# Performance work log

Measured on AMD Instinct MI355X. Metric: run time of the kernel, lower is better.

Reference implementation:

```python
import jax, jax.numpy as jnp
import numpy as np

ALPHA = 0.2  # LeakyReLU negative slope
NEG_INF = -9e15

def setup_inputs() -> dict:
    key = jax.random.key(0)
    k1, k2, k3, k4 = jax.random.split(key, 4)
    N, F_in, F_out = 8192, 256, 64
    h = jax.random.normal(k1, (N, F_in), dtype=jnp.float32)
    adj = jax.random.randint(k2, (N, N), 0, 2, dtype=jnp.int32)
    # xavier_uniform with gain=1.414
    def xavier(k, shape, gain=1.414):
        fan_in, fan_out = shape[0], shape[1]
        limit = gain * np.sqrt(6.0 / (fan_in + fan_out))
        return jax.random.uniform(k, shape, jnp.float32, -limit, limit)
    W = xavier(k3, (F_in, F_out))
    a = xavier(k4, (2 * F_out, 1))
    return {"h": h, "adj": adj, "W": W, "a": a}

def reference(h, adj, W, a):
    # Wh: (N, F_out)
    Wh = h @ W
    F_out = Wh.shape[1]
    a1 = a[:F_out, 0]   # (F_out,)
    a2 = a[F_out:, 0]   # (F_out,)
    # e_ij = LeakyReLU(Wh_i . a1 + Wh_j . a2)  -- equivalent to a^T [Wh_i || Wh_j]
    e = jax.nn.leaky_relu((Wh @ a1)[:, None] + (Wh @ a2)[None, :], negative_slope=ALPHA)
    scores = jnp.where(adj > 0, e, NEG_INF)
    attention = jax.nn.softmax(scores, axis=1)  # (N, N)
    h_prime = attention @ Wh                    # (N, F_out)
    return jax.nn.elu(h_prime)  # concat=True path
```

## Files before the change

kernel.cpp:

```cpp
#include <hip/hip_runtime.h>
#include <hip/hip_bf16.h>

#define N 8192
#define FIN 256
#define FOUT 64
#define NSLICE 8
#define SLICE_J (N / NSLICE)
#define NEG_INF -9.0e15f
#define L2E 1.4426950408889634f

typedef __attribute__((ext_vector_type(8))) short short8;
typedef __attribute__((ext_vector_type(4))) float f32x4;

static __device__ __forceinline__ short f2bf(float v) {
    __hip_bfloat16 b = __float2bfloat16(v);
    return __builtin_bit_cast(short, b);
}
static __device__ __forceinline__ float bf2f(short s) {
    unsigned u = ((unsigned)(unsigned short)s) << 16;
    return __builtin_bit_cast(float, u);
}
static __device__ __forceinline__ float exp2fast(float x) {
    return __builtin_amdgcn_exp2f(x);
}

__global__ __launch_bounds__(256) void k_wh(const float* __restrict__ h,
                                            const float* __restrict__ W,
                                            const float* __restrict__ a,
                                            float* __restrict__ Wh,
                                            float* __restrict__ s1,
                                            float* __restrict__ s2) {
    int wave = threadIdx.x >> 6, lane = threadIdx.x & 63;
    int i = blockIdx.x * 4 + wave;
    const float* hrow = h + (size_t)i * FIN;
    float acc = 0.f;
#pragma unroll 8
    for (int k = 0; k < FIN; k += 4) {
        float4 hv = *(const float4*)(hrow + k);
        acc += hv.x * W[(k + 0) * FOUT + lane];
        acc += hv.y * W[(k + 1) * FOUT + lane];
        acc += hv.z * W[(k + 2) * FOUT + lane];
        acc += hv.w * W[(k + 3) * FOUT + lane];
    }
    Wh[(size_t)i * FOUT + lane] = acc;
    float v1 = acc * a[lane];
    float v2 = acc * a[FOUT + lane];
#pragma unroll
    for (int off = 32; off; off >>= 1) {
        v1 += __shfl_xor(v1, off);
        v2 += __shfl_xor(v2, off);
    }
    if (lane == 0) { s1[i] = v1 * L2E; s2[i] = v2 * L2E; }
}

__global__ __launch_bounds__(256) void k_max(const float* __restrict__ s2,
                                             float* __restrict__ maxs2) {
    int t = threadIdx.x;
    float m = NEG_INF;
    for (int i = t; i < N; i += 256) m = fmaxf(m, s2[i]);
#pragma unroll
    for (int off = 32; off; off >>= 1) m = fmaxf(m, __shfl_xor(m, off));
    __shared__ float red[4];
    if ((t & 63) == 0) red[t >> 6] = m;
    __syncthreads();
    if (t == 0) {
        float r = fmaxf(fmaxf(red[0], red[1]), fmaxf(red[2], red[3]));
        maxs2[0] = r;
    }
}

__global__ __launch_bounds__(256) void k_repack(const float* __restrict__ Wh,
                                                short* __restrict__ WhB) {
    int t = blockIdx.x * 256 + threadIdx.x;
    int lane = t & 63, ft = (t >> 6) & 3, jt = t >> 8;
    int g = lane >> 4, r = lane & 15;
    short8 w;
#pragma unroll
    for (int q = 0; q < 8; ++q) {
        float v = Wh[(size_t)(jt * 32 + g * 8 + q) * FOUT + ft * 16 + r];
        w[q] = f2bf(v);
    }
    *((short8*)WhB + t) = w;
}

__global__ __launch_bounds__(128) void k_flash(const int* __restrict__ adj,
                                               const short* __restrict__ WhB,
                                               const float* __restrict__ s1,
                                               const float* __restrict__ s2,
                                               const float* __restrict__ maxs2,
                                               float* __restrict__ pO,
                                               float* __restrict__ pl) {
    int rb = blockIdx.x / NSLICE, sl = blockIdx.x % NSLICE;
    int wave = threadIdx.x >> 6, lane = threadIdx.x & 63;
    int r = lane & 15, g = lane >> 4;
    int row = rb * 32 + wave * 16 + r;

    __shared__ __align__(16) float s2s[SLICE_J];
    for (int t = threadIdx.x; t < SLICE_J; t += 128) s2s[t] = s2[sl * SLICE_J + t];
    __syncthreads();

    unsigned long long chunks[16];
    {
        int rbase = rb * 32 + wave * 16;
        const int* abase = adj + (size_t)rbase * N + sl * SLICE_J;
        for (int i = 0; i < 16; ++i) {
            const int* ar = abase + (size_t)i * N;
#pragma unroll
            for (int w = 0; w < 16; ++w) {
                unsigned long long bal = __ballot(ar[w * 64 + lane] > 0);
                if (r == i) chunks[w] = bal;
            }
        }
    }

    float s1i = s1[row];
    float xm = s1i + maxs2[0];
    float Mp = fmaxf(xm, 0.2f * xm);

    float l = 0.f;
    f32x4 acc0 = {0.f, 0.f, 0.f, 0.f};
    f32x4 acc1 = {0.f, 0.f, 0.f, 0.f};
    f32x4 acc2 = {0.f, 0.f, 0.f, 0.f};
    f32x4 acc3 = {0.f, 0.f, 0.f, 0.f};

#pragma unroll
    for (int step = 0; step < SLICE_J / 32; ++step) {
        unsigned bits = (unsigned)((chunks[step >> 1] >>
                                    (((step & 1) << 5) + (g << 3))) & 0xffull);
        float4 sv0 = *(const float4*)&s2s[step * 32 + g * 8];
        float4 sv1 = *(const float4*)&s2s[step * 32 + g * 8 + 4];

        short8 af;
        auto pc = [&](unsigned bit, float s2v) -> short {
            float x = s1i + s2v;
            float lr = fmaxf(x, 0.2f * x);
            float p = exp2fast(lr - Mp);
            return bit ? f2bf(p) : (short)0;
        };
        af[0] = pc(bits & 1u, sv0.x);        af[1] = pc((bits >> 1) & 1u, sv0.y);
        af[2] = pc((bits >> 2) & 1u, sv0.z); af[3] = pc((bits >> 3) & 1u, sv0.w);
        af[4] = pc((bits >> 4) & 1u, sv1.x); af[5] = pc((bits >> 5) & 1u, sv1.y);
        af[6] = pc((bits >> 6) & 1u, sv1.z); af[7] = pc((bits >> 7) & 1u, sv1.w);

        l += bf2f(af[0]) + bf2f(af[1]) + bf2f(af[2]) + bf2f(af[3]) +
             bf2f(af[4]) + bf2f(af[5]) + bf2f(af[6]) + bf2f(af[7]);

        int jt = sl * (SLICE_J / 32) + step;
        const short8* bp = (const short8*)WhB + (size_t)jt * 256 + lane;
        acc0 = __builtin_amdgcn_mfma_f32_16x16x32_bf16(af, bp[0], acc0, 0, 0, 0);
        acc1 = __builtin_amdgcn_mfma_f32_16x16x32_bf16(af, bp[64], acc1, 0, 0, 0);
        acc2 = __builtin_amdgcn_mfma_f32_16x16x32_bf16(af, bp[128], acc2, 0, 0, 0);
        acc3 = __builtin_amdgcn_mfma_f32_16x16x32_bf16(af, bp[192], acc3, 0, 0, 0);
    }

    l += __shfl_xor(l, 16);
    l += __shfl_xor(l, 32);

    int base_row = rb * 32 + wave * 16;
    f32x4 accs[4] = {acc0, acc1, acc2, acc3};
#pragma unroll
    for (int nt = 0; nt < 4; ++nt) {
#pragma unroll
        for (int reg = 0; reg < 4; ++reg) {
            int orow = base_row + g * 4 + reg;
            pO[((size_t)orow * NSLICE + sl) * FOUT + nt * 16 + r] = accs[nt][reg];
        }
    }
    if (lane < 16) pl[(size_t)row * NSLICE + sl] = l;
}

__global__ __launch_bounds__(256) void k_merge(const float* __restrict__ pO,
                                               const float* __restrict__ pl,
                                               float* __restrict__ out) {
    int t = blockIdx.x * 256 + threadIdx.x;
    int row = t >> 6, f = t & 63;
    float L = 0.f, O = 0.f;
#pragma unroll
    for (int s = 0; s < NSLICE; ++s) {
        L += pl[(size_t)row * NSLICE + s];
        O += pO[((size_t)row * NSLICE + s) * FOUT + f];
    }
    float x = O / L;
    out[t] = x > 0.f ? x : expm1f(x);
}

extern "C" void kernel_launch(void* const* d_in, const int* in_sizes, int n_in,
                              void* d_out, int out_size, void* d_ws, size_t ws_size,
                              hipStream_t stream) {
    const float* h   = (const float*)d_in[0];
    const int*   adj = (const int*)d_in[1];
    const float* W   = (const float*)d_in[2];
    const float* a   = (const float*)d_in[3];
    float* out = (float*)d_out;

    char* ws = (char*)d_ws;
    float* Wh    = (float*)ws;
    short* WhB   = (short*)(ws + (2u << 20));
    float* s1    = (float*)(ws + (3u << 20));
    float* s2    = (float*)(ws + (3u << 20) + 32768);
    float* maxs2 = (float*)(ws + (3u << 20) + 65536);
    float* pO    = (float*)(ws + (4u << 20));
    float* pl    = (float*)(ws + (20u << 20));

    k_wh<<<N / 4, 256, 0, stream>>>(h, W, a, Wh, s1, s2);
    k_max<<<1, 256, 0, stream>>>(s2, maxs2);
    k_repack<<<(N / 32) * 4 * 64 / 256, 256, 0, stream>>>(Wh, WhB);
    k_flash<<<(N / 32) * NSLICE, 128, 0, stream>>>(adj, WhB, s1, s2, maxs2, pO, pl);
    k_merge<<<N * FOUT / 256, 256, 0, stream>>>(pO, pl, out);
}
```

Baseline: 120.1 us.

## Pre-pack adjacency into bitmasks with permuted columns in a separate kernel

Adds a k_pack kernel that reads each adjacency row with 16-byte int4 loads and packs it into 64-bit ballot masks. Because of the int4 load pattern the bit order is a permuted column order, so the Wh repack and the s2 staging are remapped through realcol to match. The flash kernel then loads its masks per row directly instead of doing 16×16 scalar-load ballots with a conditional select. This trades narrow 4-byte adjacency reads for vectorized ones, at the cost of an extra launch and a round trip of the packed mask through memory.

```diff
diff --git a/kernel.cpp b/kernel.cpp
--- a/kernel.cpp
+++ b/kernel.cpp
@@ -22,6 +22,26 @@
 }
 static __device__ __forceinline__ float exp2fast(float x) {
     return __builtin_amdgcn_exp2f(x);
+}
+static __device__ __forceinline__ int realcol(int kg) {
+    return (kg & ~255) + ((kg & 63) << 2) + ((kg >> 6) & 3);
+}
+
+__global__ __launch_bounds__(256) void k_pack(const int* __restrict__ adj,
+                                              unsigned long long* __restrict__ packed) {
+    int row = (blockIdx.x * 256 + threadIdx.x) >> 6;
+    int lane = threadIdx.x & 63;
+    const int* ar = adj + (size_t)row * N;
+#pragma unroll 4
+    for (int S = 0; S < 32; ++S) {
+        int4 v = *(const int4*)(ar + S * 256 + lane * 4);
+        unsigned long long m0 = __ballot(v.x > 0);
+        unsigned long long m1 = __ballot(v.y > 0);
+        unsigned long long m2 = __ballot(v.z > 0);
+        unsigned long long m3 = __ballot(v.w > 0);
+        unsigned long long mv = lane == 0 ? m0 : lane == 1 ? m1 : lane == 2 ? m2 : m3;
+        if (lane < 4) packed[(size_t)row * 128 + S * 4 + lane] = mv;
+    }
 }
 
 __global__ __launch_bounds__(256) void k_wh(const float* __restrict__ h,
@@ -77,13 +97,14 @@
     short8 w;
 #pragma unroll
     for (int q = 0; q < 8; ++q) {
-        float v = Wh[(size_t)(jt * 32 + g * 8 + q) * FOUT + ft * 16 + r];
+        int kg = jt * 32 + g * 8 + q;
+        float v = Wh[(size_t)realcol(kg) * FOUT + ft * 16 + r];
         w[q] = f2bf(v);
     }
     *((short8*)WhB + t) = w;
 }
 
-__global__ __launch_bounds__(128) void k_flash(const int* __restrict__ adj,
+__global__ __launch_bounds__(128) void k_flash(const unsigned long long* __restrict__ packed,
                                                const short* __restrict__ WhB,
                                                const float* __restrict__ s1,
                                                const float* __restrict__ s2,
@@ -96,22 +117,22 @@
     int row = rb * 32 + wave * 16 + r;
 
     __shared__ __align__(16) float s2s[SLICE_J];
-    for (int t = threadIdx.x; t < SLICE_J; t += 128) s2s[t] = s2[sl * SLICE_J + t];
-    __syncthreads();
+    for (int t = threadIdx.x; t < SLICE_J; t += 128) {
+        int kg = sl * SLICE_J + t;
+        s2s[t] = s2[realcol(kg)];
+    }
 
     unsigned long long chunks[16];
     {
-        int rbase = rb * 32 + wave * 16;
-        const int* abase = adj + (size_t)rbase * N + sl * SLICE_J;
-        for (int i = 0; i < 16; ++i) {
-            const int* ar = abase + (size_t)i * N;
-#pragma unroll
-            for (int w = 0; w < 16; ++w) {
-                unsigned long long bal = __ballot(ar[w * 64 + lane] > 0);
-                if (r == i) chunks[w] = bal;
-            }
+        const ulonglong2* pp = (const ulonglong2*)(packed + (size_t)row * 128 + sl * 16);
+#pragma unroll
+        for (int w = 0; w < 8; ++w) {
+            ulonglong2 t2 = pp[w];
+            chunks[2 * w] = t2.x;
+            chunks[2 * w + 1] = t2.y;
         }
     }
+    __syncthreads();
 
     float s1i = s1[row];
     float xm = s1i + maxs2[0];
@@ -199,12 +220,14 @@
     float* s1    = (float*)(ws + (3u << 20));
     float* s2    = (float*)(ws + (3u << 20) + 32768);
     float* maxs2 = (float*)(ws + (3u << 20) + 65536);
-    float* pO    = (float*)(ws + (4u << 20));
-    float* pl    = (float*)(ws + (20u << 20));
-
+    unsigned long long* packed = (unsigned long long*)(ws + (4u << 20));
+    float* pO    = (float*)(ws + (16u << 20));
+    float* pl    = (float*)(ws + (32u << 20));
+
+    k_pack<<<N / 4, 256, 0, stream>>>(adj, packed);
     k_wh<<<N / 4, 256, 0, stream>>>(h, W, a, Wh, s1, s2);
     k_max<<<1, 256, 0, stream>>>(s2, maxs2);
     k_repack<<<(N / 32) * 4 * 64 / 256, 256, 0, stream>>>(Wh, WhB);
-    k_flash<<<(N / 32) * NSLICE, 128, 0, stream>>>(adj, WhB, s1, s2, maxs2, pO, pl);
+    k_flash<<<(N / 32) * NSLICE, 128, 0, stream>>>(packed, WhB, s1, s2, maxs2, pO, pl);
     k_merge<<<N * FOUT / 256, 256, 0, stream>>>(pO, pl, out);
 }
```

Result: slower. 135.2 us (+12.5%).

## Load adjacency with 128-bit nontemporal loads and permute column order

Applied to the files above, without the earlier changes.

The adjacency tile is now read with 16-byte nontemporal vector loads instead of scalar per-lane loads. Each ballot covers one component of those vectors, so the mask bits follow a permuted column order. That order is undone by remapping s2 and the repacked Wh rows through realcol(). Masks are staged in LDS rather than in 16 per-lane registers selected by r==i, which cuts register pressure and redundant selects. The cost is an LDS round trip and the added index arithmetic.

```diff
diff --git a/kernel.cpp b/kernel.cpp
--- a/kernel.cpp
+++ b/kernel.cpp
@@ -11,6 +11,8 @@
 
 typedef __attribute__((ext_vector_type(8))) short short8;
 typedef __attribute__((ext_vector_type(4))) float f32x4;
+typedef __attribute__((ext_vector_type(4))) int iv4;
+typedef unsigned long long u64;
 
 static __device__ __forceinline__ short f2bf(float v) {
     __hip_bfloat16 b = __float2bfloat16(v);
@@ -22,6 +24,9 @@
 }
 static __device__ __forceinline__ float exp2fast(float x) {
     return __builtin_amdgcn_exp2f(x);
+}
+static __device__ __forceinline__ int realcol(int kg) {
+    return (kg & ~255) + ((kg & 63) << 2) + ((kg >> 6) & 3);
 }
 
 __global__ __launch_bounds__(256) void k_wh(const float* __restrict__ h,
@@ -77,7 +82,8 @@
     short8 w;
 #pragma unroll
     for (int q = 0; q < 8; ++q) {
-        float v = Wh[(size_t)(jt * 32 + g * 8 + q) * FOUT + ft * 16 + r];
+        int kg = jt * 32 + g * 8 + q;
+        float v = Wh[(size_t)realcol(kg) * FOUT + ft * 16 + r];
         w[q] = f2bf(v);
     }
     *((short8*)WhB + t) = w;
@@ -96,22 +102,51 @@
     int row = rb * 32 + wave * 16 + r;
 
     __shared__ __align__(16) float s2s[SLICE_J];
-    for (int t = threadIdx.x; t < SLICE_J; t += 128) s2s[t] = s2[sl * SLICE_J + t];
-    __syncthreads();
-
-    unsigned long long chunks[16];
-    {
-        int rbase = rb * 32 + wave * 16;
-        const int* abase = adj + (size_t)rbase * N + sl * SLICE_J;
-        for (int i = 0; i < 16; ++i) {
-            const int* ar = abase + (size_t)i * N;
-#pragma unroll
-            for (int w = 0; w < 16; ++w) {
-                unsigned long long bal = __ballot(ar[w * 64 + lane] > 0);
-                if (r == i) chunks[w] = bal;
+    __shared__ u64 ldsm[32][17];
+
+    for (int t = threadIdx.x; t < SLICE_J; t += 128) {
+        s2s[t] = s2[realcol(sl * SLICE_J + t)];
+    }
+
+    const int* abase = adj + (size_t)(rb * 32 + wave * 16) * N + sl * SLICE_J;
+    for (int ii = 0; ii < 8; ++ii) {
+        const iv4* p0 = (const iv4*)(abase + (size_t)(2 * ii) * N) + lane;
+        const iv4* p1 = (const iv4*)(abase + (size_t)(2 * ii + 1) * N) + lane;
+        iv4 a0 = __builtin_nontemporal_load(p0);
+        iv4 a1 = __builtin_nontemporal_load(p0 + 64);
+        iv4 a2 = __builtin_nontemporal_load(p0 + 128);
+        iv4 a3 = __builtin_nontemporal_load(p0 + 192);
+        iv4 b0 = __builtin_nontemporal_load(p1);
+        iv4 b1 = __builtin_nontemporal_load(p1 + 64);
+        iv4 b2 = __builtin_nontemporal_load(p1 + 128);
+        iv4 b3 = __builtin_nontemporal_load(p1 + 192);
+        int lr0 = wave * 16 + 2 * ii, lr1 = lr0 + 1;
+        iv4 A[4] = {a0, a1, a2, a3};
+        iv4 B[4] = {b0, b1, b2, b3};
+#pragma unroll
+        for (int k = 0; k < 4; ++k) {
+            u64 m0 = __ballot(A[k][0] > 0);
+            u64 m1 = __ballot(A[k][1] > 0);
+            u64 m2 = __ballot(A[k][2] > 0);
+            u64 m3 = __ballot(A[k][3] > 0);
+            if (lane == 0) {
+                ldsm[lr0][k * 4 + 0] = m0; ldsm[lr0][k * 4 + 1] = m1;
+                ldsm[lr0][k * 4 + 2] = m2; ldsm[lr0][k * 4 + 3] = m3;
             }
         }
-    }
+#pragma unroll
+        for (int k = 0; k < 4; ++k) {
+            u64 m0 = __ballot(B[k][0] > 0);
+            u64 m1 = __ballot(B[k][1] > 0);
+            u64 m2 = __ballot(B[k][2] > 0);
+            u64 m3 = __ballot(B[k][3] > 0);
+            if (lane == 0) {
+                ldsm[lr1][k * 4 + 0] = m0; ldsm[lr1][k * 4 + 1] = m1;
+                ldsm[lr1][k * 4 + 2] = m2; ldsm[lr1][k * 4 + 3] = m3;
+            }
+        }
+    }
+    __syncthreads();
 
     float s1i = s1[row];
     float xm = s1i + maxs2[0];
@@ -123,10 +158,12 @@
     f32x4 acc2 = {0.f, 0.f, 0.f, 0.f};
     f32x4 acc3 = {0.f, 0.f, 0.f, 0.f};
 
+    const u64* mrow = &ldsm[wave * 16 + r][0];
+
 #pragma unroll
     for (int step = 0; step < SLICE_J / 32; ++step) {
-        unsigned bits = (unsigned)((chunks[step >> 1] >>
-                                    (((step & 1) << 5) + (g << 3))) & 0xffull);
+        u64 ch = mrow[step >> 1];
+        unsigned bits = (unsigned)((ch >> (((step & 1) << 5) + (g << 3))) & 0xffull);
         float4 sv0 = *(const float4*)&s2s[step * 32 + g * 8];
         float4 sv1 = *(const float4*)&s2s[step * 32 + g * 8 + 4];
 
```

Result: faster. 115.4 us (-3.9%).

## Stream adjacency with 8-byte nontemporal loads, permute columns, fuse max into repack

Applied to the files above, without the earlier changes.

Each lane now reads the adjacency matrix as int2 nontemporal loads, and the column ordering of WhB and s2 is permuted (realcol2) so the paired ballots map onto the MFMA k-layout. Adjacency loading is software-pipelined: the next 128-column chunk is prefetched while the current chunk runs its exp and MFMA work, replacing the old upfront ballot pass over all 16 rows. The separate max-reduction kernel is folded into block 0 of the repack kernel, which saves one launch. The trade-off is more registers for the prefetch buffers and more complex index mapping.

```diff
diff --git a/kernel.cpp b/kernel.cpp
--- a/kernel.cpp
+++ b/kernel.cpp
@@ -11,6 +11,8 @@
 
 typedef __attribute__((ext_vector_type(8))) short short8;
 typedef __attribute__((ext_vector_type(4))) float f32x4;
+typedef __attribute__((ext_vector_type(2))) int iv2;
+typedef unsigned long long u64;
 
 static __device__ __forceinline__ short f2bf(float v) {
     __hip_bfloat16 b = __float2bfloat16(v);
@@ -22,6 +24,9 @@
 }
 static __device__ __forceinline__ float exp2fast(float x) {
     return __builtin_amdgcn_exp2f(x);
+}
+static __device__ __forceinline__ int realcol2(int kg) {
+    return (kg & ~127) + ((kg & 63) << 1) + ((kg >> 6) & 1);
 }
 
 __global__ __launch_bounds__(256) void k_wh(const float* __restrict__ h,
@@ -53,34 +58,34 @@
     if (lane == 0) { s1[i] = v1 * L2E; s2[i] = v2 * L2E; }
 }
 
-__global__ __launch_bounds__(256) void k_max(const float* __restrict__ s2,
-                                             float* __restrict__ maxs2) {
-    int t = threadIdx.x;
-    float m = NEG_INF;
-    for (int i = t; i < N; i += 256) m = fmaxf(m, s2[i]);
-#pragma unroll
-    for (int off = 32; off; off >>= 1) m = fmaxf(m, __shfl_xor(m, off));
-    __shared__ float red[4];
-    if ((t & 63) == 0) red[t >> 6] = m;
-    __syncthreads();
-    if (t == 0) {
-        float r = fmaxf(fmaxf(red[0], red[1]), fmaxf(red[2], red[3]));
-        maxs2[0] = r;
-    }
-}
-
 __global__ __launch_bounds__(256) void k_repack(const float* __restrict__ Wh,
-                                                short* __restrict__ WhB) {
+                                                short* __restrict__ WhB,
+                                                const float* __restrict__ s2,
+                                                float* __restrict__ maxs2) {
     int t = blockIdx.x * 256 + threadIdx.x;
     int lane = t & 63, ft = (t >> 6) & 3, jt = t >> 8;
     int g = lane >> 4, r = lane & 15;
     short8 w;
 #pragma unroll
     for (int q = 0; q < 8; ++q) {
-        float v = Wh[(size_t)(jt * 32 + g * 8 + q) * FOUT + ft * 16 + r];
+        int kg = jt * 32 + g * 8 + q;
+        float v = Wh[(size_t)realcol2(kg) * FOUT + ft * 16 + r];
         w[q] = f2bf(v);
     }
     *((short8*)WhB + t) = w;
+
+    if (blockIdx.x == 0) {
+        int tt = threadIdx.x;
+        float m = NEG_INF;
+        for (int i = tt; i < N; i += 256) m = fmaxf(m, s2[i]);
+#pragma unroll
+        for (int off = 32; off; off >>= 1) m = fmaxf(m, __shfl_xor(m, off));
+        __shared__ float red[4];
+        if ((tt & 63) == 0) red[tt >> 6] = m;
+        __syncthreads();
+        if (tt == 0)
+            maxs2[0] = fmaxf(fmaxf(red[0], red[1]), fmaxf(red[2], red[3]));
+    }
 }
 
 __global__ __launch_bounds__(128) void k_flash(const int* __restrict__ adj,
@@ -96,22 +101,9 @@
     int row = rb * 32 + wave * 16 + r;
 
     __shared__ __align__(16) float s2s[SLICE_J];
-    for (int t = threadIdx.x; t < SLICE_J; t += 128) s2s[t] = s2[sl * SLICE_J + t];
+    for (int t = threadIdx.x; t < SLICE_J; t += 128)
+        s2s[t] = s2[realcol2(sl * SLICE_J + t)];
     __syncthreads();
-
-    unsigned long long chunks[16];
-    {
-        int rbase = rb * 32 + wave * 16;
-        const int* abase = adj + (size_t)rbase * N + sl * SLICE_J;
-        for (int i = 0; i < 16; ++i) {
-            const int* ar = abase + (size_t)i * N;
-#pragma unroll
-            for (int w = 0; w < 16; ++w) {
-                unsigned long long bal = __ballot(ar[w * 64 + lane] > 0);
-                if (r == i) chunks[w] = bal;
-            }
-        }
-    }
 
     float s1i = s1[row];
     float xm = s1i + maxs2[0];
@@ -123,34 +115,59 @@
     f32x4 acc2 = {0.f, 0.f, 0.f, 0.f};
     f32x4 acc3 = {0.f, 0.f, 0.f, 0.f};
 
-#pragma unroll
-    for (int step = 0; step < SLICE_J / 32; ++step) {
-        unsigned bits = (unsigned)((chunks[step >> 1] >>
-                                    (((step & 1) << 5) + (g << 3))) & 0xffull);
-        float4 sv0 = *(const float4*)&s2s[step * 32 + g * 8];
-        float4 sv1 = *(const float4*)&s2s[step * 32 + g * 8 + 4];
-
-        short8 af;
-        auto pc = [&](unsigned bit, float s2v) -> short {
-            float x = s1i + s2v;
-            float lr = fmaxf(x, 0.2f * x);
-            float p = exp2fast(lr - Mp);
-            return bit ? f2bf(p) : (short)0;
-        };
-        af[0] = pc(bits & 1u, sv0.x);        af[1] = pc((bits >> 1) & 1u, sv0.y);
-        af[2] = pc((bits >> 2) & 1u, sv0.z); af[3] = pc((bits >> 3) & 1u, sv0.w);
-        af[4] = pc((bits >> 4) & 1u, sv1.x); af[5] = pc((bits >> 5) & 1u, sv1.y);
-        af[6] = pc((bits >> 6) & 1u, sv1.z); af[7] = pc((bits >> 7) & 1u, sv1.w);
-
-        l += bf2f(af[0]) + bf2f(af[1]) + bf2f(af[2]) + bf2f(af[3]) +
-             bf2f(af[4]) + bf2f(af[5]) + bf2f(af[6]) + bf2f(af[7]);
-
-        int jt = sl * (SLICE_J / 32) + step;
-        const short8* bp = (const short8*)WhB + (size_t)jt * 256 + lane;
-        acc0 = __builtin_amdgcn_mfma_f32_16x16x32_bf16(af, bp[0], acc0, 0, 0, 0);
-        acc1 = __builtin_amdgcn_mfma_f32_16x16x32_bf16(af, bp[64], acc1, 0, 0, 0);
-        acc2 = __builtin_amdgcn_mfma_f32_16x16x32_bf16(af, bp[128], acc2, 0, 0, 0);
-        acc3 = __builtin_amdgcn_mfma_f32_16x16x32_bf16(af, bp[192], acc3, 0, 0, 0);
+    const int* abase = adj + (size_t)(rb * 32 + wave * 16) * N + sl * SLICE_J;
+
+    iv2 v[16];
+#pragma unroll
+    for (int i = 0; i < 16; ++i)
+        v[i] = __builtin_nontemporal_load((const iv2*)(abase + (size_t)i * N) + lane);
+
+#pragma unroll
+    for (int t = 0; t < 8; ++t) {
+        u64 m0, m1;
+#pragma unroll
+        for (int i = 0; i < 16; ++i) {
+            u64 b0 = __ballot(v[i][0] > 0);
+            u64 b1 = __ballot(v[i][1] > 0);
+            if (r == i) { m0 = b0; m1 = b1; }
+        }
+        if (t < 7) {
+#pragma unroll
+            for (int i = 0; i < 16; ++i)
+                v[i] = __builtin_nontemporal_load(
+                    (const iv2*)(abase + (size_t)i * N + (t + 1) * 128) + lane);
+        }
+        u64 mm[2] = {m0, m1};
+#pragma unroll
+        for (int s = 0; s < 4; ++s) {
+            unsigned bits = (unsigned)((mm[s >> 1] >>
+                                        (((s & 1) << 5) + (g << 3))) & 0xffull);
+            int S = t * 4 + s;
+            float4 sv0 = *(const float4*)&s2s[S * 32 + g * 8];
+            float4 sv1 = *(const float4*)&s2s[S * 32 + g * 8 + 4];
+
+            short8 af;
+            auto pc = [&](unsigned bit, float s2v) -> short {
+                float x = s1i + s2v;
+                float lr = fmaxf(x, 0.2f * x);
+                float p = exp2fast(lr - Mp);
+                return bit ? f2bf(p) : (short)0;
+            };
+            af[0] = pc(bits & 1u, sv0.x);        af[1] = pc((bits >> 1) & 1u, sv0.y);
+            af[2] = pc((bits >> 2) & 1u, sv0.z); af[3] = pc((bits >> 3) & 1u, sv0.w);
+            af[4] = pc((bits >> 4) & 1u, sv1.x); af[5] = pc((bits >> 5) & 1u, sv1.y);
+            af[6] = pc((bits >> 6) & 1u, sv1.z); af[7] = pc((bits >> 7) & 1u, sv1.w);
+
+            l += bf2f(af[0]) + bf2f(af[1]) + bf2f(af[2]) + bf2f(af[3]) +
+                 bf2f(af[4]) + bf2f(af[5]) + bf2f(af[6]) + bf2f(af[7]);
+
+            int jt = sl * 32 + S;
+            const short8* bp = (const short8*)WhB + (size_t)jt * 256 + lane;
+            acc0 = __builtin_amdgcn_mfma_f32_16x16x32_bf16(af, bp[0], acc0, 0, 0, 0);
+            acc1 = __builtin_amdgcn_mfma_f32_16x16x32_bf16(af, bp[64], acc1, 0, 0, 0);
+            acc2 = __builtin_amdgcn_mfma_f32_16x16x32_bf16(af, bp[128], acc2, 0, 0, 0);
+            acc3 = __builtin_amdgcn_mfma_f32_16x16x32_bf16(af, bp[192], acc3, 0, 0, 0);
+        }
     }
 
     l += __shfl_xor(l, 16);
@@ -203,8 +220,7 @@
     float* pl    = (float*)(ws + (20u << 20));
 
     k_wh<<<N / 4, 256, 0, stream>>>(h, W, a, Wh, s1, s2);
-    k_max<<<1, 256, 0, stream>>>(s2, maxs2);
-    k_repack<<<(N / 32) * 4 * 64 / 256, 256, 0, stream>>>(Wh, WhB);
+    k_repack<<<(N / 32) * 4 * 64 / 256, 256, 0, stream>>>(Wh, WhB, s2, maxs2);
     k_flash<<<(N / 32) * NSLICE, 128, 0, stream>>>(adj, WhB, s1, s2, maxs2, pO, pl);
     k_merge<<<N * FOUT / 256, 256, 0, stream>>>(pO, pl, out);
 }
```

New measurement: 123.5 us. 2.8% more time.
